# Performance work log

Measured on AMD Instinct MI355X. Metric: run time of the kernel, lower is better.

Reference implementation:

```python
import jax, jax.numpy as jnp
import numpy as np

VOCAB, EMB, CLASSES = 100000, 128, 1000
B, L = 16384, 200


def setup_inputs() -> dict:
    key = jax.random.key(0)
    k1, k2, k3, k4 = jax.random.split(key, 4)
    seq = jax.random.randint(k1, (B, L), 0, VOCAB, dtype=jnp.int64) if jax.config.jax_enable_x64 else jax.random.randint(k1, (B, L), 0, VOCAB).astype(jnp.int32)
    emb_table = jax.random.normal(k2, (VOCAB, EMB), dtype=jnp.float32) * 0.02
    fc_w = jax.random.normal(k3, (CLASSES, EMB), dtype=jnp.float32) * 0.02
    fc_b = jax.random.normal(k4, (CLASSES,), dtype=jnp.float32) * 0.02
    return {"seq": seq, "emb_table": emb_table, "fc_w": fc_w, "fc_b": fc_b}


def reference(seq, emb_table, fc_w, fc_b):
    # Masked embedding-bag (sum pool): tokens with id 0 are padding and excluded,
    # exactly matching the original nonzero-gather-sum loop.
    mask = (seq != 0).astype(emb_table.dtype)          # [B, L]
    gathered = emb_table[seq]                          # [B, L, E]
    pooled = jnp.einsum("ble,bl->be", gathered, mask)  # [B, E] sum over valid tokens
    return pooled @ fc_w.T + fc_b                      # [B, C]
```

## Files before the change

kernel.cpp:

```cpp
#include <hip/hip_runtime.h>

#define VOCAB   100000
#define EMB     128
#define CLASSES 1000
#define BATCH   16384
#define SEQLEN  200

typedef short bf16x8 __attribute__((ext_vector_type(8)));
typedef float f32x4  __attribute__((ext_vector_type(4)));

__device__ __forceinline__ unsigned short f32_to_bf16(float f) {
    unsigned int u = __builtin_bit_cast(unsigned int, f);
    u += 0x7fffu + ((u >> 16) & 1u);
    return (unsigned short)(u >> 16);
}
__device__ __forceinline__ float bf_lo(unsigned int p) { return __builtin_bit_cast(float, p << 16); }
__device__ __forceinline__ float bf_hi(unsigned int p) { return __builtin_bit_cast(float, p & 0xffff0000u); }
__device__ __forceinline__ float sb(unsigned int w, int sh) {
    return (float)(int)(signed char)((w >> sh) & 0xffu);
}

__global__ __launch_bounds__(256) void convert_emb_i8(const float* __restrict__ emb,
                                                      const float* __restrict__ fcw,
                                                      unsigned char* __restrict__ e8,
                                                      float* __restrict__ scl,
                                                      unsigned short* __restrict__ wb) {
    if (blockIdx.x < 6250) {
        const int row = blockIdx.x * 16 + (threadIdx.x >> 4);
        const int c8  = (threadIdx.x & 15) * 8;
        const float* r = emb + (long)row * EMB + c8;
        float4 v0 = *(const float4*)(r);
        float4 v1 = *(const float4*)(r + 4);
        float m = fmaxf(fmaxf(fmaxf(fabsf(v0.x), fabsf(v0.y)), fmaxf(fabsf(v0.z), fabsf(v0.w))),
                        fmaxf(fmaxf(fabsf(v1.x), fabsf(v1.y)), fmaxf(fabsf(v1.z), fabsf(v1.w))));
        m = fmaxf(m, __shfl_xor(m, 1));
        m = fmaxf(m, __shfl_xor(m, 2));
        m = fmaxf(m, __shfl_xor(m, 4));
        m = fmaxf(m, __shfl_xor(m, 8));
        const float inv = (m > 0.f) ? 127.0f / m : 0.f;
#define Q(x) ((int)fminf(fmaxf(__builtin_rintf((x) * inv), -127.f), 127.f))
        int q0 = Q(v0.x), q1 = Q(v0.y), q2 = Q(v0.z), q3 = Q(v0.w);
        int q4 = Q(v1.x), q5 = Q(v1.y), q6 = Q(v1.z), q7 = Q(v1.w);
#undef Q
        uint2 o;
        o.x = (unsigned int)(q0 & 255) | ((unsigned int)(q1 & 255) << 8) |
              ((unsigned int)(q2 & 255) << 16) | ((unsigned int)(q3 & 255) << 24);
        o.y = (unsigned int)(q4 & 255) | ((unsigned int)(q5 & 255) << 8) |
              ((unsigned int)(q6 & 255) << 16) | ((unsigned int)(q7 & 255) << 24);
        *(uint2*)(e8 + (long)row * EMB + c8) = o;
        if ((threadIdx.x & 15) == 0) scl[row] = m * (1.0f / 127.0f);
    } else {
        long i = (((long)blockIdx.x - 6250) * 256 + threadIdx.x) * 8;
        if (i >= (long)CLASSES * EMB) return;
        float4 v0 = *(const float4*)(fcw + i);
        float4 v1 = *(const float4*)(fcw + i + 4);
        uint4 o;
        o.x = (unsigned int)f32_to_bf16(v0.x) | ((unsigned int)f32_to_bf16(v0.y) << 16);
        o.y = (unsigned int)f32_to_bf16(v0.z) | ((unsigned int)f32_to_bf16(v0.w) << 16);
        o.z = (unsigned int)f32_to_bf16(v1.x) | ((unsigned int)f32_to_bf16(v1.y) << 16);
        o.w = (unsigned int)f32_to_bf16(v1.z) | ((unsigned int)f32_to_bf16(v1.w) << 16);
        *(uint4*)(wb + i) = o;
    }
}

__global__ __launch_bounds__(256) void pool_gemm_i8(const int* __restrict__ seq,
                                                    const unsigned char* __restrict__ e8,
                                                    const float* __restrict__ scl,
                                                    const unsigned short* __restrict__ fcw,
                                                    const float* __restrict__ fcb,
                                                    float* __restrict__ out) {
    __shared__ unsigned short Asub[16][136];

    const int lane = threadIdx.x & 63;
    const int wid  = threadIdx.x >> 6;
    const int quad = lane >> 4;
    const int dsub = (lane & 15) * 8;
    const int bbase = blockIdx.x * 16;

#define ISSUE(IDS, G, T, U, S)                                                \
    T = __shfl((IDS), 4 * (G) + quad);                                        \
    U = *(const uint2*)(e8 + (long)T * EMB + dsub);                           \
    S = scl[T];
#define ACCUM(T, U, S)                                                        \
    {                                                                         \
        float ms = (T != 0) ? S : 0.0f;                                       \
        a0 += ms * sb(U.x, 0);  a1 += ms * sb(U.x, 8);                        \
        a2 += ms * sb(U.x, 16); a3 += ms * sb(U.x, 24);                       \
        a4 += ms * sb(U.y, 0);  a5 += ms * sb(U.y, 8);                        \
        a6 += ms * sb(U.y, 16); a7 += ms * sb(U.y, 24);                       \
    }
#define PIPE8(IDS, G0)                                                        \
    {                                                                         \
        int t0, t1, t2, t3, t4, t5, t6, t7;                                   \
        uint2 u0, u1, u2, u3, u4, u5, u6, u7;                                 \
        float s0, s1, s2, s3, s4, s5, s6, s7;                                 \
        ISSUE(IDS, (G0) + 0, t0, u0, s0)                                      \
        ISSUE(IDS, (G0) + 1, t1, u1, s1)                                      \
        ISSUE(IDS, (G0) + 2, t2, u2, s2)                                      \
        ISSUE(IDS, (G0) + 3, t3, u3, s3)                                      \
        ISSUE(IDS, (G0) + 4, t4, u4, s4)                                      \
        ISSUE(IDS, (G0) + 5, t5, u5, s5)                                      \
        ISSUE(IDS, (G0) + 6, t6, u6, s6)                                      \
        ISSUE(IDS, (G0) + 7, t7, u7, s7)                                      \
        ACCUM(t0, u0, s0) ACCUM(t1, u1, s1) ACCUM(t2, u2, s2) ACCUM(t3, u3, s3) \
        ACCUM(t4, u4, s4) ACCUM(t5, u5, s5) ACCUM(t6, u6, s6) ACCUM(t7, u7, s7) \
    }

#pragma unroll 1
    for (int j = 0; j < 4; ++j) {
        const int bagLocal = wid * 4 + j;
        const int* srow = seq + (long)(bbase + bagLocal) * SEQLEN;
        int ids0 = srow[lane];
        int ids1 = srow[lane + 64];
        int ids2 = srow[lane + 128];
        int ids3 = (lane < 8) ? srow[lane + 192] : 0;

        float a0 = 0.f, a1 = 0.f, a2 = 0.f, a3 = 0.f;
        float a4 = 0.f, a5 = 0.f, a6 = 0.f, a7 = 0.f;

        PIPE8(ids0, 0)
        PIPE8(ids0, 8)
        PIPE8(ids1, 0)
        PIPE8(ids1, 8)
        PIPE8(ids2, 0)
        PIPE8(ids2, 8)
        {
            int t0, t1;
            uint2 u0, u1;
            float s0, s1;
            ISSUE(ids3, 0, t0, u0, s0)
            ISSUE(ids3, 1, t1, u1, s1)
            ACCUM(t0, u0, s0) ACCUM(t1, u1, s1)
        }

        a0 += __shfl_xor(a0, 16); a1 += __shfl_xor(a1, 16);
        a2 += __shfl_xor(a2, 16); a3 += __shfl_xor(a3, 16);
        a4 += __shfl_xor(a4, 16); a5 += __shfl_xor(a5, 16);
        a6 += __shfl_xor(a6, 16); a7 += __shfl_xor(a7, 16);
        a0 += __shfl_xor(a0, 32); a1 += __shfl_xor(a1, 32);
        a2 += __shfl_xor(a2, 32); a3 += __shfl_xor(a3, 32);
        a4 += __shfl_xor(a4, 32); a5 += __shfl_xor(a5, 32);
        a6 += __shfl_xor(a6, 32); a7 += __shfl_xor(a7, 32);

        if (lane < 16) {
            uint4 o;
            o.x = (unsigned int)f32_to_bf16(a0) | ((unsigned int)f32_to_bf16(a1) << 16);
            o.y = (unsigned int)f32_to_bf16(a2) | ((unsigned int)f32_to_bf16(a3) << 16);
            o.z = (unsigned int)f32_to_bf16(a4) | ((unsigned int)f32_to_bf16(a5) << 16);
            o.w = (unsigned int)f32_to_bf16(a6) | ((unsigned int)f32_to_bf16(a7) << 16);
            *(uint4*)(&Asub[bagLocal][dsub]) = o;
        }
    }
#undef PIPE8
#undef ACCUM
#undef ISSUE

    __syncthreads();

    const int arow = lane & 15;
    bf16x8 A0 = *(const bf16x8*)(&Asub[arow][quad * 8 + 0]);
    bf16x8 A1 = *(const bf16x8*)(&Asub[arow][quad * 8 + 32]);
    bf16x8 A2 = *(const bf16x8*)(&Asub[arow][quad * 8 + 64]);
    bf16x8 A3 = *(const bf16x8*)(&Asub[arow][quad * 8 + 96]);

    const int koff = quad * 8;
    int t = wid;
    int cc = t * 16 + (lane & 15);
    const unsigned short* wr = fcw + (long)((cc < CLASSES) ? cc : 0) * EMB + koff;
    bf16x8 w0 = *(const bf16x8*)(wr + 0 * 32);
    bf16x8 w1 = *(const bf16x8*)(wr + 1 * 32);
    bf16x8 w2 = *(const bf16x8*)(wr + 2 * 32);
    bf16x8 w3 = *(const bf16x8*)(wr + 3 * 32);

#pragma unroll 1
    while (t < 63) {
        bf16x8 c0 = w0, c1 = w1, c2 = w2, c3 = w3;
        const int ccNow = cc;
        t += 4;
        if (t < 63) {
            cc = t * 16 + (lane & 15);
            const unsigned short* wn = fcw + (long)((cc < CLASSES) ? cc : 0) * EMB + koff;
            w0 = *(const bf16x8*)(wn + 0 * 32);
            w1 = *(const bf16x8*)(wn + 1 * 32);
            w2 = *(const bf16x8*)(wn + 2 * 32);
            w3 = *(const bf16x8*)(wn + 3 * 32);
        }
        f32x4 acc = {0.f, 0.f, 0.f, 0.f};
        acc = __builtin_amdgcn_mfma_f32_16x16x32_bf16(A0, c0, acc, 0, 0, 0);
        acc = __builtin_amdgcn_mfma_f32_16x16x32_bf16(A1, c1, acc, 0, 0, 0);
        acc = __builtin_amdgcn_mfma_f32_16x16x32_bf16(A2, c2, acc, 0, 0, 0);
        acc = __builtin_amdgcn_mfma_f32_16x16x32_bf16(A3, c3, acc, 0, 0, 0);

        if (ccNow < CLASSES) {
            const float bias = fcb[ccNow];
            float* orow = out + (long)(bbase + quad * 4) * CLASSES + ccNow;
#pragma unroll
            for (int r = 0; r < 4; ++r)
                orow[(long)r * CLASSES] = acc[r] + bias;
        }
    }
}

__global__ __launch_bounds__(256) void convert_fcw(const float* __restrict__ fcw,
                                                   unsigned short* __restrict__ wb) {
    long i = ((long)blockIdx.x * 256 + threadIdx.x) * 8;
    if (i >= (long)CLASSES * EMB) return;
    float4 v0 = *(const float4*)(fcw + i);
    float4 v1 = *(const float4*)(fcw + i + 4);
    uint4 o;
    o.x = (unsigned int)f32_to_bf16(v0.x) | ((unsigned int)f32_to_bf16(v0.y) << 16);
    o.y = (unsigned int)f32_to_bf16(v0.z) | ((unsigned int)f32_to_bf16(v0.w) << 16);
    o.z = (unsigned int)f32_to_bf16(v1.x) | ((unsigned int)f32_to_bf16(v1.y) << 16);
    o.w = (unsigned int)f32_to_bf16(v1.z) | ((unsigned int)f32_to_bf16(v1.w) << 16);
    *(uint4*)(wb + i) = o;
}

__global__ __launch_bounds__(256) void bag_pool_f32(const int* __restrict__ seq,
                                                    const float* __restrict__ emb,
                                                    unsigned short* __restrict__ pooled) {
    const int lane = threadIdx.x & 63;
    const int wid  = threadIdx.x >> 6;
    const int b    = blockIdx.x * 4 + wid;
    const int* srow = seq + (long)b * SEQLEN;
    int ids0 = srow[lane];
    int ids1 = srow[lane + 64];
    int ids2 = srow[lane + 128];
    int ids3 = (lane < 8) ? srow[lane + 192] : 0;
    const int half = lane >> 5;
    const int dsub = (lane & 31) * 4;
    float4 acc = {0.f, 0.f, 0.f, 0.f};
#define PAIR_BODY(IDS, Q)                                                   \
    {                                                                       \
        int tok = __shfl((IDS), 2 * (Q) + half);                            \
        if (tok != 0) {                                                     \
            float4 v = *(const float4*)(emb + (long)tok * EMB + dsub);      \
            acc.x += v.x; acc.y += v.y; acc.z += v.z; acc.w += v.w;         \
        }                                                                   \
    }
#pragma unroll 8
    for (int q = 0; q < 32; ++q) PAIR_BODY(ids0, q)
#pragma unroll 8
    for (int q = 0; q < 32; ++q) PAIR_BODY(ids1, q)
#pragma unroll 8
    for (int q = 0; q < 32; ++q) PAIR_BODY(ids2, q)
#pragma unroll
    for (int q = 0; q < 4; ++q)  PAIR_BODY(ids3, q)
#undef PAIR_BODY
    acc.x += __shfl_xor(acc.x, 32);
    acc.y += __shfl_xor(acc.y, 32);
    acc.z += __shfl_xor(acc.z, 32);
    acc.w += __shfl_xor(acc.w, 32);
    if (lane < 32) {
        uint2 o;
        o.x = (unsigned int)f32_to_bf16(acc.x) | ((unsigned int)f32_to_bf16(acc.y) << 16);
        o.y = (unsigned int)f32_to_bf16(acc.z) | ((unsigned int)f32_to_bf16(acc.w) << 16);
        *(uint2*)(pooled + (long)b * EMB + dsub) = o;
    }
}

__global__ __launch_bounds__(256) void bow_gemm(const unsigned short* __restrict__ pooled,
                                                const unsigned short* __restrict__ fcw,
                                                const float* __restrict__ fcb,
                                                float* __restrict__ out) {
    const int lane = threadIdx.x & 63;
    const int wid  = threadIdx.x >> 6;
    const int quad = lane >> 4;
    const int m0   = blockIdx.x * 64 + wid * 16;
    const int mrow = m0 + (lane & 15);
    const int koff = quad * 8;

    const unsigned short* ar = pooled + (long)mrow * EMB + koff;
    bf16x8 a0 = *(const bf16x8*)(ar + 0 * 32);
    bf16x8 a1 = *(const bf16x8*)(ar + 1 * 32);
    bf16x8 a2 = *(const bf16x8*)(ar + 2 * 32);
    bf16x8 a3 = *(const bf16x8*)(ar + 3 * 32);

    int ccur = (blockIdx.y * 21) * 16 + (lane & 15);
    const unsigned short* wr = fcw + (long)((ccur < CLASSES) ? ccur : 0) * EMB + koff;
    bf16x8 w0 = *(const bf16x8*)(wr + 0 * 32);
    bf16x8 w1 = *(const bf16x8*)(wr + 1 * 32);
    bf16x8 w2 = *(const bf16x8*)(wr + 2 * 32);
    bf16x8 w3 = *(const bf16x8*)(wr + 3 * 32);

#pragma unroll 1
    for (int i = 0; i < 21; ++i) {
        bf16x8 c0 = w0, c1 = w1, c2 = w2, c3 = w3;
        const int cc = ccur;
        if (i + 1 < 21) {
            ccur += 16;
            const unsigned short* wn = fcw + (long)((ccur < CLASSES) ? ccur : 0) * EMB + koff;
            w0 = *(const bf16x8*)(wn + 0 * 32);
            w1 = *(const bf16x8*)(wn + 1 * 32);
            w2 = *(const bf16x8*)(wn + 2 * 32);
            w3 = *(const bf16x8*)(wn + 3 * 32);
        }
        f32x4 acc = {0.f, 0.f, 0.f, 0.f};
        acc = __builtin_amdgcn_mfma_f32_16x16x32_bf16(a0, c0, acc, 0, 0, 0);
        acc = __builtin_amdgcn_mfma_f32_16x16x32_bf16(a1, c1, acc, 0, 0, 0);
        acc = __builtin_amdgcn_mfma_f32_16x16x32_bf16(a2, c2, acc, 0, 0, 0);
        acc = __builtin_amdgcn_mfma_f32_16x16x32_bf16(a3, c3, acc, 0, 0, 0);

        if (cc < CLASSES) {
            const float bias = fcb[cc];
            float* orow = out + (long)(m0 + quad * 4) * CLASSES + cc;
#pragma unroll
            for (int r = 0; r < 4; ++r)
                orow[(long)r * CLASSES] = acc[r] + bias;
        }
    }
}

extern "C" void kernel_launch(void* const* d_in, const int* in_sizes, int n_in,
                              void* d_out, int out_size, void* d_ws, size_t ws_size,
                              hipStream_t stream) {
    const int*   seq = (const int*)d_in[0];
    const float* emb = (const float*)d_in[1];
    const float* fcw = (const float*)d_in[2];
    const float* fcb = (const float*)d_in[3];
    float*       out = (float*)d_out;

    float*          scl      = (float*)d_ws;
    unsigned char*  e8       = (unsigned char*)(scl + VOCAB);
    unsigned short* fcw_bf16 = (unsigned short*)(e8 + (long)VOCAB * EMB);

    const size_t need = (size_t)VOCAB * 4 + (size_t)VOCAB * EMB + (size_t)CLASSES * EMB * 2;

    if (ws_size >= need) {
        convert_emb_i8<<<6313, 256, 0, stream>>>(emb, fcw, e8, scl, fcw_bf16);
        pool_gemm_i8<<<BATCH / 16, 256, 0, stream>>>(seq, e8, scl, fcw_bf16, fcb, out);
    } else {
        unsigned short* pooled  = (unsigned short*)d_ws;
        unsigned short* fcw_bf  = pooled + (long)BATCH * EMB;
        convert_fcw<<<63, 256, 0, stream>>>(fcw, fcw_bf);
        bag_pool_f32<<<BATCH / 4, 256, 0, stream>>>(seq, emb, pooled);
        bow_gemm<<<dim3(BATCH / 64, 3), 256, 0, stream>>>(pooled, fcw_bf, fcb, out);
    }
}
```

Measured before the change: 183.1 us.

## Stage GEMM output tile in shared memory for coalesced float4 stores

Each wave now computes a 16x64 output tile (four 16x16 MFMA tiles) and writes it to a per-wave LDS buffer. It then reads the tile back and emits coalesced float4 global stores, replacing the scattered 4-byte strided row writes. This is meant to cut the number of store transactions on the 64 MB output write. The W-load software prefetch is dropped, launch bounds now request 4 blocks per SM, and about 16 KB of extra LDS per block may limit occupancy. The gcol<CLASSES check assumes CLASSES is a multiple of 4, which holds since it is 1000.

```diff
diff --git a/kernel.cpp b/kernel.cpp
--- a/kernel.cpp
+++ b/kernel.cpp
@@ -63,13 +63,14 @@
     }
 }
 
-__global__ __launch_bounds__(256) void pool_gemm_i8(const int* __restrict__ seq,
-                                                    const unsigned char* __restrict__ e8,
-                                                    const float* __restrict__ scl,
-                                                    const unsigned short* __restrict__ fcw,
-                                                    const float* __restrict__ fcb,
-                                                    float* __restrict__ out) {
+__global__ __launch_bounds__(256, 4) void pool_gemm_i8(const int* __restrict__ seq,
+                                                       const unsigned char* __restrict__ e8,
+                                                       const float* __restrict__ scl,
+                                                       const unsigned short* __restrict__ fcw,
+                                                       const float* __restrict__ fcb,
+                                                       float* __restrict__ out) {
     __shared__ unsigned short Asub[16][136];
+    __shared__ float Crep[4][16][64];
 
     const int lane = threadIdx.x & 63;
     const int wid  = threadIdx.x >> 6;
@@ -164,39 +165,35 @@
     bf16x8 A3 = *(const bf16x8*)(&Asub[arow][quad * 8 + 96]);
 
     const int koff = quad * 8;
-    int t = wid;
-    int cc = t * 16 + (lane & 15);
-    const unsigned short* wr = fcw + (long)((cc < CLASSES) ? cc : 0) * EMB + koff;
-    bf16x8 w0 = *(const bf16x8*)(wr + 0 * 32);
-    bf16x8 w1 = *(const bf16x8*)(wr + 1 * 32);
-    bf16x8 w2 = *(const bf16x8*)(wr + 2 * 32);
-    bf16x8 w3 = *(const bf16x8*)(wr + 3 * 32);
-
 #pragma unroll 1
-    while (t < 63) {
-        bf16x8 c0 = w0, c1 = w1, c2 = w2, c3 = w3;
-        const int ccNow = cc;
-        t += 4;
-        if (t < 63) {
-            cc = t * 16 + (lane & 15);
-            const unsigned short* wn = fcw + (long)((cc < CLASSES) ? cc : 0) * EMB + koff;
-            w0 = *(const bf16x8*)(wn + 0 * 32);
-            w1 = *(const bf16x8*)(wn + 1 * 32);
-            w2 = *(const bf16x8*)(wn + 2 * 32);
-            w3 = *(const bf16x8*)(wn + 3 * 32);
-        }
-        f32x4 acc = {0.f, 0.f, 0.f, 0.f};
-        acc = __builtin_amdgcn_mfma_f32_16x16x32_bf16(A0, c0, acc, 0, 0, 0);
-        acc = __builtin_amdgcn_mfma_f32_16x16x32_bf16(A1, c1, acc, 0, 0, 0);
-        acc = __builtin_amdgcn_mfma_f32_16x16x32_bf16(A2, c2, acc, 0, 0, 0);
-        acc = __builtin_amdgcn_mfma_f32_16x16x32_bf16(A3, c3, acc, 0, 0, 0);
-
-        if (ccNow < CLASSES) {
-            const float bias = fcb[ccNow];
-            float* orow = out + (long)(bbase + quad * 4) * CLASSES + ccNow;
+    for (int g = wid; g < 16; g += 4) {
+#pragma unroll
+        for (int j = 0; j < 4; ++j) {
+            const int cc = (g * 4 + j) * 16 + (lane & 15);
+            const unsigned short* wr = fcw + (long)((cc < CLASSES) ? cc : 0) * EMB + koff;
+            bf16x8 w0 = *(const bf16x8*)(wr + 0 * 32);
+            bf16x8 w1 = *(const bf16x8*)(wr + 1 * 32);
+            bf16x8 w2 = *(const bf16x8*)(wr + 2 * 32);
+            bf16x8 w3 = *(const bf16x8*)(wr + 3 * 32);
+            f32x4 acc = {0.f, 0.f, 0.f, 0.f};
+            acc = __builtin_amdgcn_mfma_f32_16x16x32_bf16(A0, w0, acc, 0, 0, 0);
+            acc = __builtin_amdgcn_mfma_f32_16x16x32_bf16(A1, w1, acc, 0, 0, 0);
+            acc = __builtin_amdgcn_mfma_f32_16x16x32_bf16(A2, w2, acc, 0, 0, 0);
+            acc = __builtin_amdgcn_mfma_f32_16x16x32_bf16(A3, w3, acc, 0, 0, 0);
+            const float bias = (cc < CLASSES) ? fcb[cc] : 0.f;
 #pragma unroll
             for (int r = 0; r < 4; ++r)
-                orow[(long)r * CLASSES] = acc[r] + bias;
+                Crep[wid][quad * 4 + r][j * 16 + (lane & 15)] = acc[r] + bias;
+        }
+        asm volatile("s_waitcnt lgkmcnt(0)" ::: "memory");
+#pragma unroll
+        for (int it = 0; it < 4; ++it) {
+            const int rr = it * 4 + (lane >> 4);
+            const int c4 = (lane & 15) * 4;
+            float4 v = *(const float4*)&Crep[wid][rr][c4];
+            const int gcol = g * 64 + c4;
+            if (gcol < CLASSES)
+                *(float4*)(out + (long)(bbase + rr) * CLASSES + gcol) = v;
         }
     }
 }
```

Measured after the change: 183.6 us. No clear change (+0.3%).

## Enlarge pool-GEMM block to 64 bags so each weight tile feeds four MFMAs

Applied to the files above, without the earlier changes.

The fused pool+GEMM kernel now uses 512-thread blocks covering 64 bags instead of 16. Each wave pools 8 bags, and in the GEMM phase every loaded fc_w tile is reused across four 16-row A tiles, cutting weight reloads per output by four. The trade-off is fewer blocks (256 instead of 1024), higher register pressure from 16 A fragments plus 4 accumulators, and more shared memory per block, which may reduce occupancy and latency hiding in the gather phase.

```diff
diff --git a/kernel.cpp b/kernel.cpp
--- a/kernel.cpp
+++ b/kernel.cpp
@@ -63,19 +63,19 @@
     }
 }
 
-__global__ __launch_bounds__(256) void pool_gemm_i8(const int* __restrict__ seq,
-                                                    const unsigned char* __restrict__ e8,
-                                                    const float* __restrict__ scl,
-                                                    const unsigned short* __restrict__ fcw,
-                                                    const float* __restrict__ fcb,
-                                                    float* __restrict__ out) {
-    __shared__ unsigned short Asub[16][136];
+__global__ __launch_bounds__(512, 2) void pool_gemm_i8(const int* __restrict__ seq,
+                                                       const unsigned char* __restrict__ e8,
+                                                       const float* __restrict__ scl,
+                                                       const unsigned short* __restrict__ fcw,
+                                                       const float* __restrict__ fcb,
+                                                       float* __restrict__ out) {
+    __shared__ unsigned short Asub[64][136];
 
     const int lane = threadIdx.x & 63;
     const int wid  = threadIdx.x >> 6;
     const int quad = lane >> 4;
     const int dsub = (lane & 15) * 8;
-    const int bbase = blockIdx.x * 16;
+    const int bbase = blockIdx.x * 64;
 
 #define ISSUE(IDS, G, T, U, S)                                                \
     T = __shfl((IDS), 4 * (G) + quad);                                        \
@@ -107,8 +107,8 @@
     }
 
 #pragma unroll 1
-    for (int j = 0; j < 4; ++j) {
-        const int bagLocal = wid * 4 + j;
+    for (int j = 0; j < 8; ++j) {
+        const int bagLocal = wid * 8 + j;
         const int* srow = seq + (long)(bbase + bagLocal) * SEQLEN;
         int ids0 = srow[lane];
         int ids1 = srow[lane + 64];
@@ -158,12 +158,15 @@
     __syncthreads();
 
     const int arow = lane & 15;
-    bf16x8 A0 = *(const bf16x8*)(&Asub[arow][quad * 8 + 0]);
-    bf16x8 A1 = *(const bf16x8*)(&Asub[arow][quad * 8 + 32]);
-    bf16x8 A2 = *(const bf16x8*)(&Asub[arow][quad * 8 + 64]);
-    bf16x8 A3 = *(const bf16x8*)(&Asub[arow][quad * 8 + 96]);
-
     const int koff = quad * 8;
+#define LDA(Aa, ROWOFF)                                                        \
+    bf16x8 Aa##0 = *(const bf16x8*)(&Asub[(ROWOFF) + arow][koff + 0]);         \
+    bf16x8 Aa##1 = *(const bf16x8*)(&Asub[(ROWOFF) + arow][koff + 32]);        \
+    bf16x8 Aa##2 = *(const bf16x8*)(&Asub[(ROWOFF) + arow][koff + 64]);        \
+    bf16x8 Aa##3 = *(const bf16x8*)(&Asub[(ROWOFF) + arow][koff + 96]);
+    LDA(A0_, 0) LDA(A1_, 16) LDA(A2_, 32) LDA(A3_, 48)
+#undef LDA
+
     int t = wid;
     int cc = t * 16 + (lane & 15);
     const unsigned short* wr = fcw + (long)((cc < CLASSES) ? cc : 0) * EMB + koff;
@@ -176,7 +179,7 @@
     while (t < 63) {
         bf16x8 c0 = w0, c1 = w1, c2 = w2, c3 = w3;
         const int ccNow = cc;
-        t += 4;
+        t += 8;
         if (t < 63) {
             cc = t * 16 + (lane & 15);
             const unsigned short* wn = fcw + (long)((cc < CLASSES) ? cc : 0) * EMB + koff;
@@ -185,18 +188,40 @@
             w2 = *(const bf16x8*)(wn + 2 * 32);
             w3 = *(const bf16x8*)(wn + 3 * 32);
         }
-        f32x4 acc = {0.f, 0.f, 0.f, 0.f};
-        acc = __builtin_amdgcn_mfma_f32_16x16x32_bf16(A0, c0, acc, 0, 0, 0);
-        acc = __builtin_amdgcn_mfma_f32_16x16x32_bf16(A1, c1, acc, 0, 0, 0);
-        acc = __builtin_amdgcn_mfma_f32_16x16x32_bf16(A2, c2, acc, 0, 0, 0);
-        acc = __builtin_amdgcn_mfma_f32_16x16x32_bf16(A3, c3, acc, 0, 0, 0);
+        f32x4 acc0 = {0.f, 0.f, 0.f, 0.f};
+        f32x4 acc1 = {0.f, 0.f, 0.f, 0.f};
+        f32x4 acc2 = {0.f, 0.f, 0.f, 0.f};
+        f32x4 acc3 = {0.f, 0.f, 0.f, 0.f};
+        acc0 = __builtin_amdgcn_mfma_f32_16x16x32_bf16(A0_0, c0, acc0, 0, 0, 0);
+        acc1 = __builtin_amdgcn_mfma_f32_16x16x32_bf16(A1_0, c0, acc1, 0, 0, 0);
+        acc2 = __builtin_amdgcn_mfma_f32_16x16x32_bf16(A2_0, c0, acc2, 0, 0, 0);
+        acc3 = __builtin_amdgcn_mfma_f32_16x16x32_bf16(A3_0, c0, acc3, 0, 0, 0);
+        acc0 = __builtin_amdgcn_mfma_f32_16x16x32_bf16(A0_1, c1, acc0, 0, 0, 0);
+        acc1 = __builtin_amdgcn_mfma_f32_16x16x32_bf16(A1_1, c1, acc1, 0, 0, 0);
+        acc2 = __builtin_amdgcn_mfma_f32_16x16x32_bf16(A2_1, c1, acc2, 0, 0, 0);
+        acc3 = __builtin_amdgcn_mfma_f32_16x16x32_bf16(A3_1, c1, acc3, 0, 0, 0);
+        acc0 = __builtin_amdgcn_mfma_f32_16x16x32_bf16(A0_2, c2, acc0, 0, 0, 0);
+        acc1 = __builtin_amdgcn_mfma_f32_16x16x32_bf16(A1_2, c2, acc1, 0, 0, 0);
+        acc2 = __builtin_amdgcn_mfma_f32_16x16x32_bf16(A2_2, c2, acc2, 0, 0, 0);
+        acc3 = __builtin_amdgcn_mfma_f32_16x16x32_bf16(A3_2, c2, acc3, 0, 0, 0);
+        acc0 = __builtin_amdgcn_mfma_f32_16x16x32_bf16(A0_3, c3, acc0, 0, 0, 0);
+        acc1 = __builtin_amdgcn_mfma_f32_16x16x32_bf16(A1_3, c3, acc1, 0, 0, 0);
+        acc2 = __builtin_amdgcn_mfma_f32_16x16x32_bf16(A2_3, c3, acc2, 0, 0, 0);
+        acc3 = __builtin_amdgcn_mfma_f32_16x16x32_bf16(A3_3, c3, acc3, 0, 0, 0);
 
         if (ccNow < CLASSES) {
             const float bias = fcb[ccNow];
-            float* orow = out + (long)(bbase + quad * 4) * CLASSES + ccNow;
+            float* orow0 = out + (long)(bbase +  0 + quad * 4) * CLASSES + ccNow;
+            float* orow1 = out + (long)(bbase + 16 + quad * 4) * CLASSES + ccNow;
+            float* orow2 = out + (long)(bbase + 32 + quad * 4) * CLASSES + ccNow;
+            float* orow3 = out + (long)(bbase + 48 + quad * 4) * CLASSES + ccNow;
 #pragma unroll
-            for (int r = 0; r < 4; ++r)
-                orow[(long)r * CLASSES] = acc[r] + bias;
+            for (int r = 0; r < 4; ++r) {
+                orow0[(long)r * CLASSES] = acc0[r] + bias;
+                orow1[(long)r * CLASSES] = acc1[r] + bias;
+                orow2[(long)r * CLASSES] = acc2[r] + bias;
+                orow3[(long)r * CLASSES] = acc3[r] + bias;
+            }
         }
     }
 }
@@ -327,7 +352,7 @@
 
     if (ws_size >= need) {
         convert_emb_i8<<<6313, 256, 0, stream>>>(emb, fcw, e8, scl, fcw_bf16);
-        pool_gemm_i8<<<BATCH / 16, 256, 0, stream>>>(seq, e8, scl, fcw_bf16, fcb, out);
+        pool_gemm_i8<<<BATCH / 64, 512, 0, stream>>>(seq, e8, scl, fcw_bf16, fcb, out);
     } else {
         unsigned short* pooled  = (unsigned short*)d_ws;
         unsigned short* fcw_bf  = pooled + (long)BATCH * EMB;
```

Result: faster. 169.2 us (-7.6%).
